# Kernel tuning notes

Hardware: AMD Instinct MI355X
Metric: run time of the kernel (lower is better)

The kernel has to match this reference:

```python
import jax, jax.numpy as jnp
import numpy as np

N = 100000
E = 1600000
DIMS = [64, 64, 64, 32]  # input -> hidden -> hidden -> num_classes
NEG_SLOPE = 0.01  # F.leaky_relu default


def setup_inputs() -> dict:
    key = jax.random.key(0)
    ks = jax.random.split(key, 8)
    inp = {
        "x": jax.random.normal(ks[0], (N, DIMS[0]), dtype=jnp.float32),
        "edge_index": jax.random.randint(ks[1], (2, E), 0, N, dtype=jnp.int64),
    }
    # GCNConv linear weights (glorot-ish scale) and biases
    for i in range(3):
        d_in, d_out = DIMS[i], DIMS[i + 1]
        scale = (2.0 / (d_in + d_out)) ** 0.5
        inp[f"W{i+1}"] = jax.random.normal(ks[2 + i], (d_in, d_out), dtype=jnp.float32) * scale
        inp[f"b{i+1}"] = jnp.zeros((d_out,), dtype=jnp.float32)
    return inp


def _gcn_conv(x, src, dst, norm, W, b):
    # x' = D^-1/2 (A+I) D^-1/2 (x W) + b
    h = x @ W                                   # [N, d_out]
    msg = h[src] * norm[:, None]                # gather + edge scaling  [E+N, d_out]
    out = jax.ops.segment_sum(msg, dst, num_segments=N)  # scatter-add
    return out + b


def reference(x, edge_index, W1, b1, W2, b2, W3, b3):
    loops = jnp.arange(N, dtype=edge_index.dtype)
    src = jnp.concatenate([edge_index[0], loops])  # add self-loops
    dst = jnp.concatenate([edge_index[1], loops])
    deg = jax.ops.segment_sum(jnp.ones_like(src, dtype=x.dtype), dst, num_segments=N)
    deg_isqrt = jax.lax.rsqrt(deg)              # deg >= 1 due to self-loops
    norm = deg_isqrt[src] * deg_isqrt[dst]      # [E+N]

    embeddings = []
    h = x
    for i, (W, b) in enumerate([(W1, b1), (W2, b2), (W3, b3)]):
        h = _gcn_conv(h, src, dst, norm, W, b)
        if i < 2:
            h = jnp.where(h >= 0, h, NEG_SLOPE * h)  # leaky_relu
        embeddings.append(h)
    return tuple(embeddings)
```

## Files before the change

### kernel.cpp

```cpp
#include <hip/hip_runtime.h>
#include <hip/hip_bf16.h>

typedef __hip_bfloat16 bf16;
typedef __attribute__((ext_vector_type(8))) short bf16x8;
typedef __attribute__((ext_vector_type(4))) short bf16x4;
typedef __attribute__((ext_vector_type(4))) float f32x4;

constexpr int BLK = 256;
constexpr int SCAN2_T = 512;
constexpr int NBLK = 400;

__device__ inline float s2f(short s) {
    union { unsigned u; float f; } z;
    z.u = ((unsigned)(unsigned short)s) << 16;
    return z.f;
}
__device__ inline short f2s(float f) {
    union { bf16 h; short s; } u;
    u.h = __float2bfloat16(f);
    return u.s;
}

__global__ void bucket_hist(const int* __restrict__ dst, int* __restrict__ blockhist,
                            int E, int EPB, int NB) {
    __shared__ int h[512];
    for (int i = threadIdx.x; i < NB; i += BLK) h[i] = 0;
    __syncthreads();
    int lo = blockIdx.x * EPB;
    int hi = min(E, lo + EPB);
    for (int t = lo + threadIdx.x; t < hi; t += BLK)
        atomicAdd(&h[dst[t] >> 8], 1);
    __syncthreads();
    for (int i = threadIdx.x; i < NB; i += BLK)
        blockhist[i * NBLK + blockIdx.x] = h[i];
}

__global__ void colscan_kernel(int* __restrict__ blockhist, int* __restrict__ btotal) {
    __shared__ int s[SCAN2_T];
    int b = blockIdx.x;
    int t = threadIdx.x;
    int v = (t < NBLK) ? blockhist[b * NBLK + t] : 0;
    s[t] = v;
    __syncthreads();
    for (int off = 1; off < SCAN2_T; off <<= 1) {
        int add = (t >= off) ? s[t - off] : 0;
        __syncthreads();
        s[t] += add;
        __syncthreads();
    }
    if (t < NBLK) blockhist[b * NBLK + t] = s[t] - v;
    if (t == SCAN2_T - 1) btotal[b] = s[SCAN2_T - 1];
}

__global__ void scan2_kernel(int* __restrict__ bsum, int nb) {
    __shared__ int s[SCAN2_T];
    int t = threadIdx.x;
    int v = (t < nb) ? bsum[t] : 0;
    s[t] = v;
    __syncthreads();
    for (int off = 1; off < SCAN2_T; off <<= 1) {
        int add = (t >= off) ? s[t - off] : 0;
        __syncthreads();
        s[t] += add;
        __syncthreads();
    }
    if (t < nb) bsum[t] = s[t] - v;
}

__global__ void bucket_scatter(const int* __restrict__ src, const int* __restrict__ dst,
                               const int* __restrict__ blockhist, const int* __restrict__ bbase,
                               int* __restrict__ ssd, int E, int EPB, int NB) {
    __shared__ int h[512];
    for (int i = threadIdx.x; i < NB; i += BLK)
        h[i] = bbase[i] + blockhist[i * NBLK + blockIdx.x];
    __syncthreads();
    int lo = blockIdx.x * EPB;
    int hi = min(E, lo + EPB);
    for (int t = lo + threadIdx.x; t < hi; t += BLK) {
        int d = dst[t];
        int pos = atomicAdd(&h[d >> 8], 1);
        ssd[pos] = (src[t] << 8) | (d & 255);
    }
}

__global__ void bucket_csr(const int* __restrict__ ssd, const int* __restrict__ bbase,
                           int* __restrict__ col, int* __restrict__ deg,
                           int* __restrict__ row_ptr, float* __restrict__ dinv,
                           int N, int E, int NB) {
    __shared__ int dloc[256];
    __shared__ int ss[256];
    __shared__ int cur[256];
    int b = blockIdx.x;
    int t = threadIdx.x;
    int lo = bbase[b];
    int hi = (b + 1 < NB) ? bbase[b + 1] : E;
    dloc[t] = 0;
    __syncthreads();
    for (int j = lo + t; j < hi; j += BLK)
        atomicAdd(&dloc[ssd[j] & 255], 1);
    __syncthreads();
    int own = dloc[t];
    ss[t] = own;
    __syncthreads();
    for (int off = 1; off < 256; off <<= 1) {
        int add = (t >= off) ? ss[t - off] : 0;
        __syncthreads();
        ss[t] += add;
        __syncthreads();
    }
    int excl = ss[t] - own;
    cur[t] = lo + excl;
    int node = (b << 8) + t;
    if (node < N) {
        deg[node] = own;
        row_ptr[node] = lo + excl;
        dinv[node] = rsqrtf((float)own + 1.0f);
    }
    __syncthreads();
    for (int j = lo + t; j < hi; j += BLK) {
        unsigned e = (unsigned)ssd[j];
        int p = atomicAdd(&cur[e & 255], 1);
        col[p] = (int)(e >> 8);
    }
}

__global__ void wconv_all(const float* __restrict__ W1, const float* __restrict__ W2,
                          const float* __restrict__ W3, bf16* __restrict__ WT1,
                          bf16* __restrict__ WT2, bf16* __restrict__ WT3) {
    int idx = blockIdx.x * blockDim.x + threadIdx.x;
    if (idx < 4096) {
        int k = idx >> 6, c = idx & 63;
        WT1[c * 64 + k] = __float2bfloat16(W1[idx]);
    } else if (idx < 8192) {
        int i = idx - 4096, k = i >> 6, c = i & 63;
        WT2[c * 64 + k] = __float2bfloat16(W2[i]);
    } else if (idx < 10240) {
        int i = idx - 8192, k = i >> 5, c = i & 31;
        WT3[c * 64 + k] = __float2bfloat16(W3[i]);
    }
}

template <int DOUT, bool AF32>
__global__ void mfma_gemm(const void* __restrict__ inv, const bf16* __restrict__ WT,
                          const float* __restrict__ dinv, bf16* __restrict__ hlin, int n) {
    constexpr int NT = DOUT / 16;
    const int lane = threadIdx.x & 63;
    const int wave = threadIdx.x >> 6;
    const int q = lane >> 4;
    const int l16 = lane & 15;
    const int row0 = blockIdx.x * 64 + wave * 16;

    int arow = row0 + l16;
    if (arow >= n) arow = n - 1;

    bf16x8 a0, a1;
    if (AF32) {
        const float* in = (const float*)inv;
        const float* p = in + (size_t)arow * 64 + q * 8;
        float4 f0 = *(const float4*)(p);
        float4 f1 = *(const float4*)(p + 4);
        float4 g0 = *(const float4*)(p + 32);
        float4 g1 = *(const float4*)(p + 36);
        bf16 t0[8] = {__float2bfloat16(f0.x), __float2bfloat16(f0.y), __float2bfloat16(f0.z), __float2bfloat16(f0.w),
                      __float2bfloat16(f1.x), __float2bfloat16(f1.y), __float2bfloat16(f1.z), __float2bfloat16(f1.w)};
        bf16 t1[8] = {__float2bfloat16(g0.x), __float2bfloat16(g0.y), __float2bfloat16(g0.z), __float2bfloat16(g0.w),
                      __float2bfloat16(g1.x), __float2bfloat16(g1.y), __float2bfloat16(g1.z), __float2bfloat16(g1.w)};
        __builtin_memcpy(&a0, t0, 16);
        __builtin_memcpy(&a1, t1, 16);
    } else {
        const bf16* in = (const bf16*)inv;
        a0 = *(const bf16x8*)(in + (size_t)arow * 64 + q * 8);
        a1 = *(const bf16x8*)(in + (size_t)arow * 64 + 32 + q * 8);
    }

    f32x4 acc[NT];
#pragma unroll
    for (int ct = 0; ct < NT; ++ct) {
        const bf16* wrow = WT + (size_t)(ct * 16 + l16) * 64 + q * 8;
        bf16x8 b0 = *(const bf16x8*)(wrow);
        bf16x8 b1 = *(const bf16x8*)(wrow + 32);
        f32x4 c = {0.f, 0.f, 0.f, 0.f};
        c = __builtin_amdgcn_mfma_f32_16x16x32_bf16(a0, b0, c, 0, 0, 0);
        c = __builtin_amdgcn_mfma_f32_16x16x32_bf16(a1, b1, c, 0, 0, 0);
        acc[ct] = c;
    }

    float dv[4];
#pragma unroll
    for (int r = 0; r < 4; ++r) {
        int rr = row0 + q * 4 + r;
        dv[r] = (rr < n) ? dinv[rr] : 0.0f;
    }
#pragma unroll
    for (int ct = 0; ct < NT; ++ct) {
#pragma unroll
        for (int r = 0; r < 4; ++r) {
            int rr = row0 + q * 4 + r;
            if (rr < n)
                hlin[(size_t)rr * DOUT + ct * 16 + l16] = __float2bfloat16(acc[ct][r] * dv[r]);
        }
    }
}

template <bool LEAKY>
__global__ __launch_bounds__(256, 8)
void agg64_kernel(const int* __restrict__ row_ptr, const int* __restrict__ deg,
                  const int* __restrict__ col, const bf16* __restrict__ hlin,
                  const float* __restrict__ dinv, const float* __restrict__ b,
                  float* __restrict__ out, bf16* __restrict__ actb, int n) {
    const int wid = (blockIdx.x * blockDim.x + threadIdx.x) >> 6;
    const int lane = threadIdx.x & 63;
    const int sub = lane >> 4;
    const int g = (lane >> 3) & 1;
    const int fl = lane & 7;
    const int node = wid * 4 + sub;
    const int PAD = n;

    const bool valid = node < n;
    const int nc = valid ? node : n - 1;
    const int beg = row_ptr[nc];
    const int dg = valid ? deg[nc] : 0;
    const int end = beg + dg;

    float acc[8], acc2[8];
    {
        int c0 = (valid && g == 0) ? node : PAD;
        bf16x8 sv = *(const bf16x8*)(hlin + (size_t)c0 * 64 + (fl << 3));
#pragma unroll
        for (int k = 0; k < 8; ++k) { acc[k] = s2f(sv[k]); acc2[k] = 0.0f; }
    }

    int m = dg;
    m = max(m, __shfl_xor(m, 16));
    m = max(m, __shfl_xor(m, 32));
    const int iters = (m + 7) >> 3;

    int idx = beg + g;
    int c0 = col[idx     < end ? idx     : 0];
    int c1 = col[idx + 2 < end ? idx + 2 : 0];
    int c2 = col[idx + 4 < end ? idx + 4 : 0];
    int c3 = col[idx + 6 < end ? idx + 6 : 0];
    for (int j = 0; j < iters; ++j) {
        const int a0 = (idx     < end) ? c0 : PAD;
        const int a1 = (idx + 2 < end) ? c1 : PAD;
        const int a2 = (idx + 4 < end) ? c2 : PAD;
        const int a3 = (idx + 6 < end) ? c3 : PAD;
        idx += 8;
        c0 = col[idx     < end ? idx     : 0];
        c1 = col[idx + 2 < end ? idx + 2 : 0];
        c2 = col[idx + 4 < end ? idx + 4 : 0];
        c3 = col[idx + 6 < end ? idx + 6 : 0];
        bf16x8 v0 = *(const bf16x8*)(hlin + (size_t)a0 * 64 + (fl << 3));
        bf16x8 v1 = *(const bf16x8*)(hlin + (size_t)a1 * 64 + (fl << 3));
        bf16x8 v2 = *(const bf16x8*)(hlin + (size_t)a2 * 64 + (fl << 3));
        bf16x8 v3 = *(const bf16x8*)(hlin + (size_t)a3 * 64 + (fl << 3));
#pragma unroll
        for (int k = 0; k < 8; ++k) {
            acc[k]  += s2f(v0[k]) + s2f(v1[k]);
            acc2[k] += s2f(v2[k]) + s2f(v3[k]);
        }
    }

#pragma unroll
    for (int k = 0; k < 8; ++k) acc[k] += acc2[k];
#pragma unroll
    for (int k = 0; k < 8; ++k) acc[k] += __shfl_xor(acc[k], 8);

    const float dv = dinv[nc];
    const float4 bb0 = *(const float4*)(b + (fl << 3));
    const float4 bb1 = *(const float4*)(b + (fl << 3) + 4);
    float vals[8];
    vals[0] = acc[0] * dv + bb0.x;
    vals[1] = acc[1] * dv + bb0.y;
    vals[2] = acc[2] * dv + bb0.z;
    vals[3] = acc[3] * dv + bb0.w;
    vals[4] = acc[4] * dv + bb1.x;
    vals[5] = acc[5] * dv + bb1.y;
    vals[6] = acc[6] * dv + bb1.z;
    vals[7] = acc[7] * dv + bb1.w;
    if (LEAKY) {
#pragma unroll
        for (int k = 0; k < 8; ++k) vals[k] = (vals[k] >= 0.0f) ? vals[k] : 0.01f * vals[k];
    }
    if (valid && g == 0) {
        float* op = out + (size_t)node * 64 + (fl << 3);
        f32x4 o0 = {vals[0], vals[1], vals[2], vals[3]};
        f32x4 o1 = {vals[4], vals[5], vals[6], vals[7]};
        __builtin_nontemporal_store(o0, (f32x4*)op);
        __builtin_nontemporal_store(o1, (f32x4*)(op + 4));
        if (actb) {
            bf16x8 ob;
#pragma unroll
            for (int k = 0; k < 8; ++k) ob[k] = f2s(vals[k]);
            *(bf16x8*)(actb + (size_t)node * 64 + (fl << 3)) = ob;
        }
    }
}

__global__ __launch_bounds__(256, 8)
void agg32_kernel(const int* __restrict__ row_ptr, const int* __restrict__ deg,
                  const int* __restrict__ col, const bf16* __restrict__ hlin,
                  const float* __restrict__ dinv, const float* __restrict__ b,
                  float* __restrict__ out, int n) {
    const int wid = (blockIdx.x * blockDim.x + threadIdx.x) >> 6;
    const int lane = threadIdx.x & 63;
    const int sub = lane >> 4;
    const int g = (lane >> 3) & 1;
    const int fl = lane & 7;
    const int node = wid * 4 + sub;
    const int PAD = 2 * n;

    const bool valid = node < n;
    const int nc = valid ? node : n - 1;
    const int beg = row_ptr[nc];
    const int dg = valid ? deg[nc] : 0;
    const int end = beg + dg;

    float acc[4], acc2[4];
    {
        int c0 = (valid && g == 0) ? node : PAD;
        bf16x4 sv = *(const bf16x4*)(hlin + (size_t)c0 * 32 + (fl << 2));
#pragma unroll
        for (int k = 0; k < 4; ++k) { acc[k] = s2f(sv[k]); acc2[k] = 0.0f; }
    }

    int m = dg;
    m = max(m, __shfl_xor(m, 16));
    m = max(m, __shfl_xor(m, 32));
    const int iters = (m + 7) >> 3;

    int idx = beg + g;
    int c0 = col[idx     < end ? idx     : 0];
    int c1 = col[idx + 2 < end ? idx + 2 : 0];
    int c2 = col[idx + 4 < end ? idx + 4 : 0];
    int c3 = col[idx + 6 < end ? idx + 6 : 0];
    for (int j = 0; j < iters; ++j) {
        const int a0 = (idx     < end) ? c0 : PAD;
        const int a1 = (idx + 2 < end) ? c1 : PAD;
        const int a2 = (idx + 4 < end) ? c2 : PAD;
        const int a3 = (idx + 6 < end) ? c3 : PAD;
        idx += 8;
        c0 = col[idx     < end ? idx     : 0];
        c1 = col[idx + 2 < end ? idx + 2 : 0];
        c2 = col[idx + 4 < end ? idx + 4 : 0];
        c3 = col[idx + 6 < end ? idx + 6 : 0];
        bf16x4 v0 = *(const bf16x4*)(hlin + (size_t)a0 * 32 + (fl << 2));
        bf16x4 v1 = *(const bf16x4*)(hlin + (size_t)a1 * 32 + (fl << 2));
        bf16x4 v2 = *(const bf16x4*)(hlin + (size_t)a2 * 32 + (fl << 2));
        bf16x4 v3 = *(const bf16x4*)(hlin + (size_t)a3 * 32 + (fl << 2));
#pragma unroll
        for (int k = 0; k < 4; ++k) {
            acc[k]  += s2f(v0[k]) + s2f(v1[k]);
            acc2[k] += s2f(v2[k]) + s2f(v3[k]);
        }
    }

#pragma unroll
    for (int k = 0; k < 4; ++k) acc[k] += acc2[k];
#pragma unroll
    for (int k = 0; k < 4; ++k) acc[k] += __shfl_xor(acc[k], 8);

    const float dv = dinv[nc];
    const float4 bb = *(const float4*)(b + (fl << 2));
    float vals[4];
    vals[0] = acc[0] * dv + bb.x;
    vals[1] = acc[1] * dv + bb.y;
    vals[2] = acc[2] * dv + bb.z;
    vals[3] = acc[3] * dv + bb.w;
    if (valid && g == 0) {
        f32x4 o = {vals[0], vals[1], vals[2], vals[3]};
        __builtin_nontemporal_store(o, (f32x4*)(out + (size_t)node * 32 + (fl << 2)));
    }
}

extern "C" void kernel_launch(void* const* d_in, const int* in_sizes, int n_in,
                              void* d_out, int out_size, void* d_ws, size_t ws_size,
                              hipStream_t stream) {
    const float* x  = (const float*)d_in[0];
    const int*   ei = (const int*)d_in[1];
    const float* W1 = (const float*)d_in[2];
    const float* b1 = (const float*)d_in[3];
    const float* W2 = (const float*)d_in[4];
    const float* b2 = (const float*)d_in[5];
    const float* W3 = (const float*)d_in[6];
    const float* b3 = (const float*)d_in[7];
    float* out = (float*)d_out;

    const int N = in_sizes[0] / 64;
    const int E = in_sizes[1] / 2;
    const int* src = ei;
    const int* dst = ei + E;

    const int NB  = (N + 255) >> 8;
    const int EPB = (E + NBLK - 1) / NBLK;

    char* w = (char*)d_ws;
    auto take = [&](size_t bytes) { char* p = w; w += (bytes + 15) & ~(size_t)15; return p; };
    int*   col       = (int*)take((size_t)E * 4);
    int*   ssd       = (int*)take((size_t)E * 4);
    bf16*  hlin      = (bf16*)take(((size_t)N * 64 + 64) * 2);
    bf16*  actb      = (bf16*)take((size_t)N * 64 * 2);
    bf16*  WT1       = (bf16*)take(64 * 64 * 2);
    bf16*  WT2       = (bf16*)take(64 * 64 * 2);
    bf16*  WT3       = (bf16*)take(32 * 64 * 2);
    int*   deg       = (int*)take((size_t)N * 4);
    int*   row_ptr   = (int*)take((size_t)N * 4);
    float* dinv      = (float*)take((size_t)N * 4);
    int*   blockhist = (int*)take((size_t)NB * NBLK * 4);
    int*   btotal    = (int*)take((size_t)SCAN2_T * 4);

    float* out0 = out;
    float* out1 = out + (size_t)N * 64;
    float* out2 = out + (size_t)N * 128;

    const int gemmBlocks = (N + 63) / 64;
    const int aggWaves = (N + 3) / 4;
    const int aggBlocks = (aggWaves * 64 + BLK - 1) / BLK;

    hipMemsetAsync(hlin + (size_t)N * 64, 0, 128, stream);

    bucket_hist<<<NBLK, BLK, 0, stream>>>(dst, blockhist, E, EPB, NB);
    colscan_kernel<<<NB, SCAN2_T, 0, stream>>>(blockhist, btotal);
    scan2_kernel<<<1, SCAN2_T, 0, stream>>>(btotal, NB);
    bucket_scatter<<<NBLK, BLK, 0, stream>>>(src, dst, blockhist, btotal, ssd, E, EPB, NB);
    bucket_csr<<<NB, BLK, 0, stream>>>(ssd, btotal, col, deg, row_ptr, dinv, N, E, NB);

    wconv_all<<<40, BLK, 0, stream>>>(W1, W2, W3, WT1, WT2, WT3);

    mfma_gemm<64, true><<<gemmBlocks, BLK, 0, stream>>>(x, WT1, dinv, hlin, N);
    agg64_kernel<true><<<aggBlocks, BLK, 0, stream>>>(
        row_ptr, deg, col, hlin, dinv, b1, out0, actb, N);

    mfma_gemm<64, false><<<gemmBlocks, BLK, 0, stream>>>(actb, WT2, dinv, hlin, N);
    agg64_kernel<true><<<aggBlocks, BLK, 0, stream>>>(
        row_ptr, deg, col, hlin, dinv, b2, out1, actb, N);

    mfma_gemm<32, false><<<gemmBlocks, BLK, 0, stream>>>(actb, WT3, dinv, hlin, N);
    agg32_kernel<<<aggBlocks, BLK, 0, stream>>>(
        row_ptr, deg, col, hlin, dinv, b3, out2, N);
}
```

Measured before the change: 269.8 us.

## Fuse aggregation with next layer's MFMA GEMM via shared-memory tile

Each 64-wide aggregation block now handles 16 nodes, stages the leaky-ReLU activations as bf16 in shared memory, and immediately multiplies them by the next layer's weights with MFMA, writing the pre-scaled hidden features for the following aggregation. This removes the separate GEMM launches for layers 2 and 3 and the round trip of the bf16 activation buffer through global memory. Two ping-pong feature buffers replace the single hlin/actb pair. The cost is a block-wide barrier after the irregular gather and idle waves during the 32-wide GEMM.

```diff
diff --git a/kernel.cpp b/kernel.cpp
--- a/kernel.cpp
+++ b/kernel.cpp
@@ -202,18 +202,21 @@
     }
 }
 
-template <bool LEAKY>
+template <int DOUTN, bool LEAKY>
 __global__ __launch_bounds__(256, 8)
-void agg64_kernel(const int* __restrict__ row_ptr, const int* __restrict__ deg,
-                  const int* __restrict__ col, const bf16* __restrict__ hlin,
-                  const float* __restrict__ dinv, const float* __restrict__ b,
-                  float* __restrict__ out, bf16* __restrict__ actb, int n) {
-    const int wid = (blockIdx.x * blockDim.x + threadIdx.x) >> 6;
+void agg_gemm_kernel(const int* __restrict__ row_ptr, const int* __restrict__ deg,
+                     const int* __restrict__ col, const bf16* __restrict__ hlin,
+                     const float* __restrict__ dinv, const float* __restrict__ b,
+                     float* __restrict__ out, const bf16* __restrict__ WTn,
+                     bf16* __restrict__ hout, int n) {
+    __shared__ short tile[16 * 72];
+    const int wave = threadIdx.x >> 6;
     const int lane = threadIdx.x & 63;
     const int sub = lane >> 4;
     const int g = (lane >> 3) & 1;
     const int fl = lane & 7;
-    const int node = wid * 4 + sub;
+    const int base = blockIdx.x * 16;
+    const int node = base + wave * 4 + sub;
     const int PAD = n;
 
     const bool valid = node < n;
@@ -241,19 +244,19 @@
     int c2 = col[idx + 4 < end ? idx + 4 : 0];
     int c3 = col[idx + 6 < end ? idx + 6 : 0];
     for (int j = 0; j < iters; ++j) {
-        const int a0 = (idx     < end) ? c0 : PAD;
-        const int a1 = (idx + 2 < end) ? c1 : PAD;
-        const int a2 = (idx + 4 < end) ? c2 : PAD;
-        const int a3 = (idx + 6 < end) ? c3 : PAD;
+        const int a0i = (idx     < end) ? c0 : PAD;
+        const int a1i = (idx + 2 < end) ? c1 : PAD;
+        const int a2i = (idx + 4 < end) ? c2 : PAD;
+        const int a3i = (idx + 6 < end) ? c3 : PAD;
         idx += 8;
         c0 = col[idx     < end ? idx     : 0];
         c1 = col[idx + 2 < end ? idx + 2 : 0];
         c2 = col[idx + 4 < end ? idx + 4 : 0];
         c3 = col[idx + 6 < end ? idx + 6 : 0];
-        bf16x8 v0 = *(const bf16x8*)(hlin + (size_t)a0 * 64 + (fl << 3));
-        bf16x8 v1 = *(const bf16x8*)(hlin + (size_t)a1 * 64 + (fl << 3));
-        bf16x8 v2 = *(const bf16x8*)(hlin + (size_t)a2 * 64 + (fl << 3));
-        bf16x8 v3 = *(const bf16x8*)(hlin + (size_t)a3 * 64 + (fl << 3));
+        bf16x8 v0 = *(const bf16x8*)(hlin + (size_t)a0i * 64 + (fl << 3));
+        bf16x8 v1 = *(const bf16x8*)(hlin + (size_t)a1i * 64 + (fl << 3));
+        bf16x8 v2 = *(const bf16x8*)(hlin + (size_t)a2i * 64 + (fl << 3));
+        bf16x8 v3 = *(const bf16x8*)(hlin + (size_t)a3i * 64 + (fl << 3));
 #pragma unroll
         for (int k = 0; k < 8; ++k) {
             acc[k]  += s2f(v0[k]) + s2f(v1[k]);
@@ -282,17 +285,37 @@
 #pragma unroll
         for (int k = 0; k < 8; ++k) vals[k] = (vals[k] >= 0.0f) ? vals[k] : 0.01f * vals[k];
     }
-    if (valid && g == 0) {
-        float* op = out + (size_t)node * 64 + (fl << 3);
-        f32x4 o0 = {vals[0], vals[1], vals[2], vals[3]};
-        f32x4 o1 = {vals[4], vals[5], vals[6], vals[7]};
-        __builtin_nontemporal_store(o0, (f32x4*)op);
-        __builtin_nontemporal_store(o1, (f32x4*)(op + 4));
-        if (actb) {
-            bf16x8 ob;
-#pragma unroll
-            for (int k = 0; k < 8; ++k) ob[k] = f2s(vals[k]);
-            *(bf16x8*)(actb + (size_t)node * 64 + (fl << 3)) = ob;
+    if (g == 0) {
+        bf16x8 ob;
+#pragma unroll
+        for (int k = 0; k < 8; ++k) ob[k] = f2s(vals[k]);
+        *(bf16x8*)(tile + (wave * 4 + sub) * 72 + (fl << 3)) = ob;
+        if (valid) {
+            float* op = out + (size_t)node * 64 + (fl << 3);
+            f32x4 o0 = {vals[0], vals[1], vals[2], vals[3]};
+            f32x4 o1 = {vals[4], vals[5], vals[6], vals[7]};
+            __builtin_nontemporal_store(o0, (f32x4*)op);
+            __builtin_nontemporal_store(o1, (f32x4*)(op + 4));
+        }
+    }
+    __syncthreads();
+
+    const int q = sub;
+    const int l16 = lane & 15;
+    if (DOUTN == 64 || wave < 2) {
+        bf16x8 a0 = *(const bf16x8*)(tile + l16 * 72 + q * 8);
+        bf16x8 a1 = *(const bf16x8*)(tile + l16 * 72 + 32 + q * 8);
+        const bf16* wrow = WTn + (size_t)(wave * 16 + l16) * 64 + q * 8;
+        bf16x8 b0 = *(const bf16x8*)(wrow);
+        bf16x8 b1 = *(const bf16x8*)(wrow + 32);
+        f32x4 c = {0.f, 0.f, 0.f, 0.f};
+        c = __builtin_amdgcn_mfma_f32_16x16x32_bf16(a0, b0, c, 0, 0, 0);
+        c = __builtin_amdgcn_mfma_f32_16x16x32_bf16(a1, b1, c, 0, 0, 0);
+#pragma unroll
+        for (int r = 0; r < 4; ++r) {
+            int rr = base + q * 4 + r;
+            if (rr < n)
+                hout[(size_t)rr * DOUTN + wave * 16 + l16] = __float2bfloat16(c[r] * dinv[rr]);
         }
     }
 }
@@ -398,8 +421,8 @@
     auto take = [&](size_t bytes) { char* p = w; w += (bytes + 15) & ~(size_t)15; return p; };
     int*   col       = (int*)take((size_t)E * 4);
     int*   ssd       = (int*)take((size_t)E * 4);
-    bf16*  hlin      = (bf16*)take(((size_t)N * 64 + 64) * 2);
-    bf16*  actb      = (bf16*)take((size_t)N * 64 * 2);
+    bf16*  hlinA     = (bf16*)take(((size_t)N * 64 + 64) * 2);
+    bf16*  hlinB     = (bf16*)take(((size_t)N * 64 + 64) * 2);
     bf16*  WT1       = (bf16*)take(64 * 64 * 2);
     bf16*  WT2       = (bf16*)take(64 * 64 * 2);
     bf16*  WT3       = (bf16*)take(32 * 64 * 2);
@@ -414,10 +437,12 @@
     float* out2 = out + (size_t)N * 128;
 
     const int gemmBlocks = (N + 63) / 64;
+    const int fusedBlocks = (N + 15) / 16;
     const int aggWaves = (N + 3) / 4;
     const int aggBlocks = (aggWaves * 64 + BLK - 1) / BLK;
 
-    hipMemsetAsync(hlin + (size_t)N * 64, 0, 128, stream);
+    hipMemsetAsync(hlinA + (size_t)N * 64, 0, 128, stream);
+    hipMemsetAsync(hlinB + (size_t)N * 64, 0, 128, stream);
 
     bucket_hist<<<NBLK, BLK, 0, stream>>>(dst, blockhist, E, EPB, NB);
     colscan_kernel<<<NB, SCAN2_T, 0, stream>>>(blockhist, btotal);
@@ -427,15 +452,14 @@
 
     wconv_all<<<40, BLK, 0, stream>>>(W1, W2, W3, WT1, WT2, WT3);
 
-    mfma_gemm<64, true><<<gemmBlocks, BLK, 0, stream>>>(x, WT1, dinv, hlin, N);
-    agg64_kernel<true><<<aggBlocks, BLK, 0, stream>>>(
-        row_ptr, deg, col, hlin, dinv, b1, out0, actb, N);
-
-    mfma_gemm<64, false><<<gemmBlocks, BLK, 0, stream>>>(actb, WT2, dinv, hlin, N);
-    agg64_kernel<true><<<aggBlocks, BLK, 0, stream>>>(
-        row_ptr, deg, col, hlin, dinv, b2, out1, actb, N);
-
-    mfma_gemm<32, false><<<gemmBlocks, BLK, 0, stream>>>(actb, WT3, dinv, hlin, N);
+    mfma_gemm<64, true><<<gemmBlocks, BLK, 0, stream>>>(x, WT1, dinv, hlinA, N);
+
+    agg_gemm_kernel<64, true><<<fusedBlocks, BLK, 0, stream>>>(
+        row_ptr, deg, col, hlinA, dinv, b1, out0, WT2, hlinB, N);
+
+    agg_gemm_kernel<32, true><<<fusedBlocks, BLK, 0, stream>>>(
+        row_ptr, deg, col, hlinB, dinv, b2, out1, WT3, hlinA, N);
+
     agg32_kernel<<<aggBlocks, BLK, 0, stream>>>(
-        row_ptr, deg, col, hlin, dinv, b3, out2, N);
-}
+        row_ptr, deg, col, hlinA, dinv, b3, out2, N);
+}
```

New measurement: 260.9 us. -3.3%, faster.
